# Performance work log

Measured on AMD Instinct MI355X. Metric: run time of the kernel, lower is better.

Reference implementation:

```python
import jax, jax.numpy as jnp
import numpy as np

NH = 8          # num_heads (init kwarg)
NUM_GROUPS = 32
EPS = 1e-5


def setup_inputs() -> dict:
    key = jax.random.key(0)
    ks = jax.random.split(key, 4)
    B, C, H, W = 2, 512, 64, 64
    x = jax.random.normal(ks[0], (B, C, H, W), dtype=jnp.float32)
    qkv_w = jax.random.normal(ks[1], (3 * C, C), dtype=jnp.float32) * (1.0 / np.sqrt(C))
    proj_w = jax.random.normal(ks[2], (C, C), dtype=jnp.float32) * (1.0 / np.sqrt(C))
    proj_b = jax.random.normal(ks[3], (C,), dtype=jnp.float32) * 0.02
    gn_w = jnp.ones((C,), dtype=jnp.float32)
    gn_b = jnp.zeros((C,), dtype=jnp.float32)
    return {"x": x, "qkv_w": qkv_w, "proj_w": proj_w, "proj_b": proj_b,
            "gn_w": gn_w, "gn_b": gn_b}


def _group_norm(x, gamma, beta):
    B, C, H, W = x.shape
    xg = x.reshape(B, NUM_GROUPS, C // NUM_GROUPS, H, W)
    mean = xg.mean(axis=(2, 3, 4), keepdims=True)
    var = xg.var(axis=(2, 3, 4), keepdims=True)
    xg = (xg - mean) * jax.lax.rsqrt(var + EPS)
    x = xg.reshape(B, C, H, W)
    return x * gamma[None, :, None, None] + beta[None, :, None, None]


def reference(x, qkv_w, proj_w, proj_b, gn_w, gn_b):
    B, C, H, W = x.shape
    h = _group_norm(x, gn_w, gn_b)
    # 1x1 conv == channel matmul
    qkv = jnp.einsum('oc,bchw->bohw', qkv_w, h)  # [B, 3C, H, W]
    # faithful legacy reshape: per-head contiguous [q,k,v] blocks of 3*C//NH channels
    qkv = qkv.reshape(B * NH, 3 * C // NH, H * W)
    q, k, v = jnp.split(qkv, 3, axis=1)          # each [B*NH, C//NH, HW]
    scale = 1.0 / np.sqrt(np.sqrt(C // NH))
    attn = jnp.einsum('bci,bcj->bij', q * scale, k * scale)  # [B*NH, HW, HW]
    attn = jax.nn.softmax(attn, axis=-1)
    hout = jnp.einsum('bij,bcj->bci', attn, v)   # [B*NH, C//NH, HW]
    hout = hout.reshape(B, C, H, W)
    hout = jnp.einsum('oc,bchw->bohw', proj_w, hout) + proj_b[None, :, None, None]
    return x + hout
```

## Files before the change

### kernel.cpp

```cpp
#include <hip/hip_runtime.h>
#include <math.h>

typedef __attribute__((ext_vector_type(8))) short short8;
typedef __attribute__((ext_vector_type(4))) float floatx4;

__device__ __forceinline__ unsigned short f2bf(float f) {
  union { float f; unsigned int u; } v; v.f = f;
  unsigned int r = v.u + 0x7fffu + ((v.u >> 16) & 1u);
  return (unsigned short)(r >> 16);
}

__device__ __forceinline__ unsigned int pack2(unsigned short a, unsigned short b) {
  return (unsigned int)a | ((unsigned int)b << 16);
}

__device__ __forceinline__ unsigned int rbits(float f) {
  union { float f; unsigned int u; } v; v.f = f;
  return v.u + 0x8000u;
}

__device__ __forceinline__ float fast_exp2(float x) {
#if __has_builtin(__builtin_amdgcn_exp2f)
  return __builtin_amdgcn_exp2f(x);
#else
  return exp2f(x);
#endif
}

__device__ __forceinline__ void async16(const unsigned short* gp, unsigned short* lp) {
  __builtin_amdgcn_global_load_lds(
      (__attribute__((address_space(1))) void*)(gp),
      (__attribute__((address_space(3))) void*)(lp), 16, 0, 0);
}

__global__ void gn_stats(const float* __restrict__ x, float* __restrict__ stats) {
  int bg = blockIdx.x;
  const float4* p = (const float4*)(x + (size_t)bg * 65536);
  float s = 0.f, ss = 0.f;
  for (int i = threadIdx.x; i < 16384; i += 256) {
    float4 v = p[i];
    s  += v.x + v.y + v.z + v.w;
    ss += v.x*v.x + v.y*v.y + v.z*v.z + v.w*v.w;
  }
  #pragma unroll
  for (int off = 32; off >= 1; off >>= 1) {
    s  += __shfl_xor(s,  off, 64);
    ss += __shfl_xor(ss, off, 64);
  }
  __shared__ float red[2][4];
  int wv = threadIdx.x >> 6;
  if ((threadIdx.x & 63) == 0) { red[0][wv] = s; red[1][wv] = ss; }
  __syncthreads();
  if (threadIdx.x == 0) {
    s  = red[0][0] + red[0][1] + red[0][2] + red[0][3];
    ss = red[1][0] + red[1][1] + red[1][2] + red[1][3];
    float mean = s * (1.f/65536.f);
    float var  = ss * (1.f/65536.f) - mean*mean;
    stats[2*bg]   = mean;
    stats[2*bg+1] = rsqrtf(var + 1e-5f);
  }
}

__global__ void gn_apply_t(const float* __restrict__ x, const float* __restrict__ stats,
                           const float* __restrict__ gw, const float* __restrict__ gb,
                           unsigned short* __restrict__ h_t) {
  __shared__ __align__(16) unsigned short tile[64][72];
  const int b = blockIdx.z, c0 = blockIdx.y * 64, hw0 = blockIdx.x * 64;
  const int t = threadIdx.x;
  {
    const int cl = t >> 2;
    const int hs = (t & 3) * 16;
    const int c  = c0 + cl;
    const int g  = c >> 4;
    const float mean = stats[2*(b*32 + g)];
    const float rstd = stats[2*(b*32 + g) + 1];
    const float w  = gw[c] * rstd;
    const float bb = gb[c] - mean * w;
    const float4* src = (const float4*)(x + ((size_t)(b*512 + c))*4096 + hw0 + hs);
    #pragma unroll
    for (int i = 0; i < 4; i++) {
      float4 vv = src[i];
      unsigned short* d = &tile[cl][hs + i*4];
      d[0] = f2bf(vv.x*w + bb); d[1] = f2bf(vv.y*w + bb);
      d[2] = f2bf(vv.z*w + bb); d[3] = f2bf(vv.w*w + bb);
    }
  }
  __syncthreads();
  {
    const int hwl = t >> 2;
    const int cs  = (t & 3) * 16;
    uint4 w0, w1;
    w0.x = pack2(tile[cs+ 0][hwl], tile[cs+ 1][hwl]);
    w0.y = pack2(tile[cs+ 2][hwl], tile[cs+ 3][hwl]);
    w0.z = pack2(tile[cs+ 4][hwl], tile[cs+ 5][hwl]);
    w0.w = pack2(tile[cs+ 6][hwl], tile[cs+ 7][hwl]);
    w1.x = pack2(tile[cs+ 8][hwl], tile[cs+ 9][hwl]);
    w1.y = pack2(tile[cs+10][hwl], tile[cs+11][hwl]);
    w1.z = pack2(tile[cs+12][hwl], tile[cs+13][hwl]);
    w1.w = pack2(tile[cs+14][hwl], tile[cs+15][hwl]);
    unsigned short* dst = h_t + ((size_t)(b*4096 + hw0 + hwl))*512 + c0 + cs;
    *(uint4*)dst       = w0;
    *(uint4*)(dst + 8) = w1;
  }
}

__global__ void castw(const float* __restrict__ src, unsigned short* __restrict__ dst, int n4) {
  int i = blockIdx.x * 256 + threadIdx.x;
  if (i < n4) {
    float4 vv = ((const float4*)src)[i];
    uint2 o;
    o.x = pack2(f2bf(vv.x), f2bf(vv.y));
    o.y = pack2(f2bf(vv.z), f2bf(vv.w));
    ((uint2*)dst)[i] = o;
  }
}

template <int MODE>
__global__ __launch_bounds__(256, 2)
void gemm_bt(const unsigned short* __restrict__ A,
             const unsigned short* __restrict__ Bt,
             unsigned short* __restrict__ q_t,
             unsigned short* __restrict__ k_t,
             unsigned short* __restrict__ v_,
             float* __restrict__ outp,
             const float* __restrict__ xres,
             const float* __restrict__ pbias) {
  __shared__ __align__(16) unsigned short As[128*32];
  __shared__ __align__(16) unsigned short Bs[128*32];
  const int b   = blockIdx.z;
  const int n0  = blockIdx.x * 128;
  const int o0  = blockIdx.y * 128;
  const int tid = threadIdx.x;
  const int wave = tid >> 6, lane = tid & 63;
  const int wr = wave >> 1, wc = wave & 1;
  const int fm = lane & 15, fq = lane >> 4;
  const int srow = lane >> 2, scol = (lane & 3) * 8;

  const unsigned short* Ab = A + (size_t)o0 * 512;
  const unsigned short* Bb = Bt + ((size_t)b*4096 + n0) * 512;

  floatx4 acc[4][4];
  #pragma unroll
  for (int i = 0; i < 4; i++)
    #pragma unroll
    for (int j = 0; j < 4; j++) acc[i][j] = (floatx4){0.f,0.f,0.f,0.f};

  for (int k0 = 0; k0 < 512; k0 += 32) {
    __syncthreads();
    #pragma unroll
    for (int cc = 0; cc < 2; cc++) {
      int ch = wave*2 + cc;
      async16(Ab + (size_t)(ch*16 + srow)*512 + k0 + scol, &As[ch*512]);
      async16(Bb + (size_t)(ch*16 + srow)*512 + k0 + scol, &Bs[ch*512]);
    }
    __syncthreads();
    short8 af[4], bf[4];
    #pragma unroll
    for (int f = 0; f < 4; f++) {
      af[f] = *(const short8*)&As[(wr*64 + f*16 + fm)*32 + fq*8];
      bf[f] = *(const short8*)&Bs[(wc*64 + f*16 + fm)*32 + fq*8];
    }
    #pragma unroll
    for (int fr = 0; fr < 4; fr++)
      #pragma unroll
      for (int fc = 0; fc < 4; fc++)
        acc[fr][fc] = __builtin_amdgcn_mfma_f32_16x16x32_bf16(af[fr], bf[fc], acc[fr][fc], 0, 0, 0);
  }

  if (MODE == 0) {
    #pragma unroll
    for (int fr = 0; fr < 4; fr++) {
      const int ob     = o0 + wr*64 + fr*16;
      const int head   = ob / 192;
      const int rem    = ob % 192;
      const int region = rem >> 6;
      const int dsub   = (rem & 63) + fq*4;
      const int bhh    = b*8 + head;
      #pragma unroll
      for (int fc = 0; fc < 4; fc++) {
        const int i = n0 + wc*64 + fc*16 + fm;
        if (region == 0) {
          unsigned short t4[4];
          #pragma unroll
          for (int r = 0; r < 4; r++) t4[r] = f2bf(acc[fr][fc][r] * 0.18033688f);
          uint2 o; o.x = pack2(t4[0], t4[1]); o.y = pack2(t4[2], t4[3]);
          *(uint2*)&q_t[((size_t)bhh*4096 + i)*64 + dsub] = o;
        } else if (region == 1) {
          unsigned short t4[4];
          #pragma unroll
          for (int r = 0; r < 4; r++) t4[r] = f2bf(acc[fr][fc][r]);
          uint2 o; o.x = pack2(t4[0], t4[1]); o.y = pack2(t4[2], t4[3]);
          *(uint2*)&k_t[((size_t)bhh*4096 + i)*64 + dsub] = o;
        } else {
          #pragma unroll
          for (int r = 0; r < 4; r++)
            v_[((size_t)bhh*64 + dsub + r)*4096 + i] = f2bf(acc[fr][fc][r]);
        }
      }
    }
  } else {
    #pragma unroll
    for (int fr = 0; fr < 4; fr++)
      #pragma unroll
      for (int fc = 0; fc < 4; fc++) {
        const int i = n0 + wc*64 + fc*16 + fm;
        #pragma unroll
        for (int r = 0; r < 4; r++) {
          const int o = o0 + wr*64 + fr*16 + fq*4 + r;
          const size_t idx = ((size_t)b*512 + o)*4096 + i;
          outp[idx] = xres[idx] + pbias[o] + acc[fr][fc][r];
        }
      }
  }
}

__global__ __launch_bounds__(256, 2)
void attn_kernel(const unsigned short* __restrict__ q_t,
                 const unsigned short* __restrict__ k_t,
                 const unsigned short* __restrict__ v_,
                 unsigned short* __restrict__ hout_t) {
  __shared__ __align__(16) unsigned short Ks[2][64*72];
  __shared__ __align__(16) unsigned short Vs[2][64*72];
  __shared__ __align__(16) unsigned short Ps[128*72];

  const int bh  = blockIdx.x;
  const int q0  = blockIdx.y * 128;
  const int tid = threadIdx.x;
  const int wave = tid >> 6, lane = tid & 63;
  const int fm = lane & 15, fq = lane >> 4;

  short8 qf[2][2];
  #pragma unroll
  for (int ih = 0; ih < 2; ih++) {
    const unsigned short* qrow = q_t + ((size_t)bh*4096 + q0 + wave*32 + ih*16 + fm)*64;
    qf[ih][0] = *(const short8*)(qrow + fq*8);
    qf[ih][1] = *(const short8*)(qrow + 32 + fq*8);
  }

  floatx4 o_acc[2][4];
  #pragma unroll
  for (int a = 0; a < 2; a++)
    #pragma unroll
    for (int d = 0; d < 4; d++) o_acc[a][d] = (floatx4){0.f,0.f,0.f,0.f};
  float l0 = 0.f, l1 = 0.f;

  const int sr = tid >> 3;
  const int sc = (tid & 7) * 8;
  const unsigned short* kbase = k_t + (size_t)bh*262144;
  const unsigned short* vbase = v_  + (size_t)bh*262144;
  unsigned short* Pw = &Ps[(wave*32)*72];

  uint4 kr0 = *(const uint4*)&kbase[(size_t)sr*64 + sc];
  uint4 kr1 = *(const uint4*)&kbase[(size_t)(sr+32)*64 + sc];
  uint4 vr0 = *(const uint4*)&vbase[(size_t)sr*4096 + sc];
  uint4 vr1 = *(const uint4*)&vbase[(size_t)(sr+32)*4096 + sc];

  for (int it = 0; it < 64; it++) {
    unsigned short* Kc = Ks[it & 1];
    unsigned short* Vc = Vs[it & 1];
    *(uint4*)&Kc[sr*72 + sc]      = kr0;
    *(uint4*)&Kc[(sr+32)*72 + sc] = kr1;
    *(uint4*)&Vc[sr*72 + sc]      = vr0;
    *(uint4*)&Vc[(sr+32)*72 + sc] = vr1;
    __syncthreads();

    {
      const int jn = ((it + 1) & 63) * 64;
      kr0 = *(const uint4*)&kbase[(size_t)(jn + sr)*64 + sc];
      kr1 = *(const uint4*)&kbase[(size_t)(jn + sr + 32)*64 + sc];
      vr0 = *(const uint4*)&vbase[(size_t)sr*4096 + jn + sc];
      vr1 = *(const uint4*)&vbase[(size_t)(sr+32)*4096 + jn + sc];
    }

    floatx4 s[4][2];
    #pragma unroll
    for (int jf = 0; jf < 4; jf++) {
      short8 kf0 = *(const short8*)&Kc[(jf*16 + fm)*72 + fq*8];
      short8 kf1 = *(const short8*)&Kc[(jf*16 + fm)*72 + 32 + fq*8];
      #pragma unroll
      for (int ih = 0; ih < 2; ih++) {
        floatx4 a = (floatx4){0.f,0.f,0.f,0.f};
        a = __builtin_amdgcn_mfma_f32_16x16x32_bf16(kf0, qf[ih][0], a, 0, 0, 0);
        a = __builtin_amdgcn_mfma_f32_16x16x32_bf16(kf1, qf[ih][1], a, 0, 0, 0);
        s[jf][ih] = a;
      }
    }

    #pragma unroll
    for (int jf = 0; jf < 4; jf++) {
      #pragma unroll
      for (int ih = 0; ih < 2; ih++) {
        float p0 = fast_exp2(s[jf][ih][0]);
        float p1 = fast_exp2(s[jf][ih][1]);
        float p2 = fast_exp2(s[jf][ih][2]);
        float p3 = fast_exp2(s[jf][ih][3]);
        if (ih) l1 += (p0 + p1) + (p2 + p3); else l0 += (p0 + p1) + (p2 + p3);
        uint2 w;
        w.x = __builtin_amdgcn_perm(rbits(p1), rbits(p0), 0x07060302u);
        w.y = __builtin_amdgcn_perm(rbits(p3), rbits(p2), 0x07060302u);
        *(uint2*)&Pw[(ih*16 + fm)*72 + jf*16 + fq*4] = w;
      }
    }

    #pragma unroll
    for (int jc = 0; jc < 2; jc++) {
      short8 pf0 = *(const short8*)&Pw[(fm)*72      + jc*32 + fq*8];
      short8 pf1 = *(const short8*)&Pw[(16 + fm)*72 + jc*32 + fq*8];
      #pragma unroll
      for (int df = 0; df < 4; df++) {
        short8 vf = *(const short8*)&Vc[(df*16 + fm)*72 + jc*32 + fq*8];
        o_acc[0][df] = __builtin_amdgcn_mfma_f32_16x16x32_bf16(pf0, vf, o_acc[0][df], 0, 0, 0);
        o_acc[1][df] = __builtin_amdgcn_mfma_f32_16x16x32_bf16(pf1, vf, o_acc[1][df], 0, 0, 0);
      }
    }
  }

  l0 += __shfl_xor(l0, 16, 64); l0 += __shfl_xor(l0, 32, 64);
  l1 += __shfl_xor(l1, 16, 64); l1 += __shfl_xor(l1, 32, 64);

  const int bb = bh >> 3;
  const int cb = (bh & 7) * 64;
  #pragma unroll
  for (int ih = 0; ih < 2; ih++) {
    #pragma unroll
    for (int r = 0; r < 4; r++) {
      const int src = (lane & 48) | (fq*4 + r);
      const float lv = __shfl(ih ? l1 : l0, src, 64);
      const float inv = 1.f / lv;
      const int i = q0 + wave*32 + ih*16 + fq*4 + r;
      #pragma unroll
      for (int df = 0; df < 4; df++)
        hout_t[((size_t)bb*4096 + i)*512 + cb + df*16 + fm] = f2bf(o_acc[ih][df][r] * inv);
    }
  }
}

extern "C" void kernel_launch(void* const* d_in, const int* in_sizes, int n_in,
                              void* d_out, int out_size, void* d_ws, size_t ws_size,
                              hipStream_t stream) {
  (void)in_sizes; (void)n_in; (void)out_size; (void)ws_size;
  const float* x      = (const float*)d_in[0];
  const float* qkv_w  = (const float*)d_in[1];
  const float* proj_w = (const float*)d_in[2];
  const float* proj_b = (const float*)d_in[3];
  const float* gn_w   = (const float*)d_in[4];
  const float* gn_b   = (const float*)d_in[5];
  float* out = (float*)d_out;

  char* ws = (char*)d_ws;
  unsigned short* h_t   = (unsigned short*)(ws);
  unsigned short* q_t   = (unsigned short*)(ws + ((size_t)8  << 20));
  unsigned short* k_t   = (unsigned short*)(ws + ((size_t)16 << 20));
  unsigned short* v_    = (unsigned short*)(ws + ((size_t)24 << 20));
  unsigned short* wqkv  = (unsigned short*)(ws + ((size_t)32 << 20));
  unsigned short* wproj = (unsigned short*)(ws + ((size_t)34 << 20));
  float* stats          = (float*)(ws + ((size_t)35 << 20));
  unsigned short* hout_t = h_t;

  gn_stats<<<dim3(64), dim3(256), 0, stream>>>(x, stats);
  gn_apply_t<<<dim3(64, 8, 2), dim3(256), 0, stream>>>(x, stats, gn_w, gn_b, h_t);
  castw<<<dim3(768), dim3(256), 0, stream>>>(qkv_w, wqkv, 196608);
  castw<<<dim3(256), dim3(256), 0, stream>>>(proj_w, wproj, 65536);
  gemm_bt<0><<<dim3(32, 12, 2), dim3(256), 0, stream>>>(wqkv, h_t, q_t, k_t, v_,
                                                        nullptr, nullptr, nullptr);
  attn_kernel<<<dim3(16, 32), dim3(256), 0, stream>>>(q_t, k_t, v_, hout_t);
  gemm_bt<1><<<dim3(32, 4, 2), dim3(256), 0, stream>>>(wproj, hout_t,
                                                       nullptr, nullptr, nullptr,
                                                       out, x, proj_b);
}
```

Before: 227.3 us.

## Use 32x32 MFMA in attention with register-resident P, vectorize V stores, merge weight casts

The attention inner loop now uses 32x32x16 MFMA for QK^T and keeps the exponentiated scores in registers, feeding them directly as the A operand of 32x32x8 MFMAs for PV. This drops the shared-memory P buffer along with its write/read round trip and cuts LDS traffic per iteration. In the QKV GEMM, the V region swaps the MFMA operands so each lane holds contiguous tokens and can issue packed 8-byte stores instead of scattered 2-byte ones. The two weight-cast launches are merged into one. The larger accumulators increase register pressure, which could hurt occupancy.

```diff
diff --git a/kernel.cpp b/kernel.cpp
--- a/kernel.cpp
+++ b/kernel.cpp
@@ -2,7 +2,9 @@
 #include <math.h>
 
 typedef __attribute__((ext_vector_type(8))) short short8;
+typedef __attribute__((ext_vector_type(4))) short short4v;
 typedef __attribute__((ext_vector_type(4))) float floatx4;
+typedef __attribute__((ext_vector_type(16))) float floatx16;
 
 __device__ __forceinline__ unsigned short f2bf(float f) {
   union { float f; unsigned int u; } v; v.f = f;
@@ -104,15 +106,17 @@
   }
 }
 
-__global__ void castw(const float* __restrict__ src, unsigned short* __restrict__ dst, int n4) {
+__global__ void castw2(const float* __restrict__ sa, unsigned short* __restrict__ da, int n4a,
+                       const float* __restrict__ sb, unsigned short* __restrict__ db) {
   int i = blockIdx.x * 256 + threadIdx.x;
-  if (i < n4) {
-    float4 vv = ((const float4*)src)[i];
-    uint2 o;
-    o.x = pack2(f2bf(vv.x), f2bf(vv.y));
-    o.y = pack2(f2bf(vv.z), f2bf(vv.w));
-    ((uint2*)dst)[i] = o;
-  }
+  const float* s; unsigned short* d;
+  if (i < n4a) { s = sa; d = da; }
+  else { i -= n4a; s = sb; d = db; }
+  float4 vv = ((const float4*)s)[i];
+  uint2 o;
+  o.x = pack2(f2bf(vv.x), f2bf(vv.y));
+  o.y = pack2(f2bf(vv.z), f2bf(vv.w));
+  ((uint2*)d)[i] = o;
 }
 
 template <int MODE>
@@ -139,6 +143,13 @@
   const unsigned short* Ab = A + (size_t)o0 * 512;
   const unsigned short* Bb = Bt + ((size_t)b*4096 + n0) * 512;
 
+  bool vsw[4];
+  #pragma unroll
+  for (int fr = 0; fr < 4; fr++) {
+    const int ob = o0 + wr*64 + fr*16;
+    vsw[fr] = (MODE == 0) && ((ob % 192) >> 6) == 2;
+  }
+
   floatx4 acc[4][4];
   #pragma unroll
   for (int i = 0; i < 4; i++)
@@ -161,10 +172,17 @@
       bf[f] = *(const short8*)&Bs[(wc*64 + f*16 + fm)*32 + fq*8];
     }
     #pragma unroll
-    for (int fr = 0; fr < 4; fr++)
-      #pragma unroll
-      for (int fc = 0; fc < 4; fc++)
-        acc[fr][fc] = __builtin_amdgcn_mfma_f32_16x16x32_bf16(af[fr], bf[fc], acc[fr][fc], 0, 0, 0);
+    for (int fr = 0; fr < 4; fr++) {
+      if (vsw[fr]) {
+        #pragma unroll
+        for (int fc = 0; fc < 4; fc++)
+          acc[fr][fc] = __builtin_amdgcn_mfma_f32_16x16x32_bf16(bf[fc], af[fr], acc[fr][fc], 0, 0, 0);
+      } else {
+        #pragma unroll
+        for (int fc = 0; fc < 4; fc++)
+          acc[fr][fc] = __builtin_amdgcn_mfma_f32_16x16x32_bf16(af[fr], bf[fc], acc[fr][fc], 0, 0, 0);
+      }
+    }
   }
 
   if (MODE == 0) {
@@ -174,27 +192,33 @@
       const int head   = ob / 192;
       const int rem    = ob % 192;
       const int region = rem >> 6;
-      const int dsub   = (rem & 63) + fq*4;
       const int bhh    = b*8 + head;
       #pragma unroll
       for (int fc = 0; fc < 4; fc++) {
-        const int i = n0 + wc*64 + fc*16 + fm;
         if (region == 0) {
+          const int i = n0 + wc*64 + fc*16 + fm;
+          const int dsub = (rem & 63) + fq*4;
           unsigned short t4[4];
           #pragma unroll
           for (int r = 0; r < 4; r++) t4[r] = f2bf(acc[fr][fc][r] * 0.18033688f);
           uint2 o; o.x = pack2(t4[0], t4[1]); o.y = pack2(t4[2], t4[3]);
           *(uint2*)&q_t[((size_t)bhh*4096 + i)*64 + dsub] = o;
         } else if (region == 1) {
+          const int i = n0 + wc*64 + fc*16 + fm;
+          const int dsub = (rem & 63) + fq*4;
           unsigned short t4[4];
           #pragma unroll
           for (int r = 0; r < 4; r++) t4[r] = f2bf(acc[fr][fc][r]);
           uint2 o; o.x = pack2(t4[0], t4[1]); o.y = pack2(t4[2], t4[3]);
           *(uint2*)&k_t[((size_t)bhh*4096 + i)*64 + dsub] = o;
         } else {
+          const int dsub = (rem & 63) + fm;
+          const int tok0 = n0 + wc*64 + fc*16 + fq*4;
+          unsigned short t4[4];
           #pragma unroll
-          for (int r = 0; r < 4; r++)
-            v_[((size_t)bhh*64 + dsub + r)*4096 + i] = f2bf(acc[fr][fc][r]);
+          for (int r = 0; r < 4; r++) t4[r] = f2bf(acc[fr][fc][r]);
+          uint2 o; o.x = pack2(t4[0], t4[1]); o.y = pack2(t4[2], t4[3]);
+          *(uint2*)&v_[((size_t)bhh*64 + dsub)*4096 + tok0] = o;
         }
       }
     }
@@ -221,34 +245,32 @@
                  unsigned short* __restrict__ hout_t) {
   __shared__ __align__(16) unsigned short Ks[2][64*72];
   __shared__ __align__(16) unsigned short Vs[2][64*72];
-  __shared__ __align__(16) unsigned short Ps[128*72];
 
   const int bh  = blockIdx.x;
   const int q0  = blockIdx.y * 128;
   const int tid = threadIdx.x;
   const int wave = tid >> 6, lane = tid & 63;
-  const int fm = lane & 15, fq = lane >> 4;
-
-  short8 qf[2][2];
-  #pragma unroll
-  for (int ih = 0; ih < 2; ih++) {
-    const unsigned short* qrow = q_t + ((size_t)bh*4096 + q0 + wave*32 + ih*16 + fm)*64;
-    qf[ih][0] = *(const short8*)(qrow + fq*8);
-    qf[ih][1] = *(const short8*)(qrow + 32 + fq*8);
-  }
-
-  floatx4 o_acc[2][4];
-  #pragma unroll
-  for (int a = 0; a < 2; a++)
-    #pragma unroll
-    for (int d = 0; d < 4; d++) o_acc[a][d] = (floatx4){0.f,0.f,0.f,0.f};
-  float l0 = 0.f, l1 = 0.f;
+  const int ln = lane & 31, h = lane >> 5;
+
+  short8 qf[4];
+  {
+    const unsigned short* qrow = q_t + ((size_t)bh*4096 + q0 + wave*32 + ln)*64;
+    #pragma unroll
+    for (int kc = 0; kc < 4; kc++)
+      qf[kc] = *(const short8*)(qrow + kc*16 + h*8);
+  }
+
+  floatx16 o_acc[2];
+  #pragma unroll
+  for (int dn = 0; dn < 2; dn++)
+    #pragma unroll
+    for (int r = 0; r < 16; r++) o_acc[dn][r] = 0.f;
+  float l = 0.f;
 
   const int sr = tid >> 3;
   const int sc = (tid & 7) * 8;
   const unsigned short* kbase = k_t + (size_t)bh*262144;
   const unsigned short* vbase = v_  + (size_t)bh*262144;
-  unsigned short* Pw = &Ps[(wave*32)*72];
 
   uint4 kr0 = *(const uint4*)&kbase[(size_t)sr*64 + sc];
   uint4 kr1 = *(const uint4*)&kbase[(size_t)(sr+32)*64 + sc];
@@ -272,66 +294,59 @@
       vr1 = *(const uint4*)&vbase[(size_t)(sr+32)*4096 + jn + sc];
     }
 
-    floatx4 s[4][2];
-    #pragma unroll
-    for (int jf = 0; jf < 4; jf++) {
-      short8 kf0 = *(const short8*)&Kc[(jf*16 + fm)*72 + fq*8];
-      short8 kf1 = *(const short8*)&Kc[(jf*16 + fm)*72 + 32 + fq*8];
-      #pragma unroll
-      for (int ih = 0; ih < 2; ih++) {
-        floatx4 a = (floatx4){0.f,0.f,0.f,0.f};
-        a = __builtin_amdgcn_mfma_f32_16x16x32_bf16(kf0, qf[ih][0], a, 0, 0, 0);
-        a = __builtin_amdgcn_mfma_f32_16x16x32_bf16(kf1, qf[ih][1], a, 0, 0, 0);
-        s[jf][ih] = a;
-      }
-    }
-
-    #pragma unroll
-    for (int jf = 0; jf < 4; jf++) {
-      #pragma unroll
-      for (int ih = 0; ih < 2; ih++) {
-        float p0 = fast_exp2(s[jf][ih][0]);
-        float p1 = fast_exp2(s[jf][ih][1]);
-        float p2 = fast_exp2(s[jf][ih][2]);
-        float p3 = fast_exp2(s[jf][ih][3]);
-        if (ih) l1 += (p0 + p1) + (p2 + p3); else l0 += (p0 + p1) + (p2 + p3);
-        uint2 w;
-        w.x = __builtin_amdgcn_perm(rbits(p1), rbits(p0), 0x07060302u);
-        w.y = __builtin_amdgcn_perm(rbits(p3), rbits(p2), 0x07060302u);
-        *(uint2*)&Pw[(ih*16 + fm)*72 + jf*16 + fq*4] = w;
-      }
-    }
-
-    #pragma unroll
-    for (int jc = 0; jc < 2; jc++) {
-      short8 pf0 = *(const short8*)&Pw[(fm)*72      + jc*32 + fq*8];
-      short8 pf1 = *(const short8*)&Pw[(16 + fm)*72 + jc*32 + fq*8];
-      #pragma unroll
-      for (int df = 0; df < 4; df++) {
-        short8 vf = *(const short8*)&Vc[(df*16 + fm)*72 + jc*32 + fq*8];
-        o_acc[0][df] = __builtin_amdgcn_mfma_f32_16x16x32_bf16(pf0, vf, o_acc[0][df], 0, 0, 0);
-        o_acc[1][df] = __builtin_amdgcn_mfma_f32_16x16x32_bf16(pf1, vf, o_acc[1][df], 0, 0, 0);
-      }
-    }
-  }
-
-  l0 += __shfl_xor(l0, 16, 64); l0 += __shfl_xor(l0, 32, 64);
-  l1 += __shfl_xor(l1, 16, 64); l1 += __shfl_xor(l1, 32, 64);
+    floatx16 st[2];
+    #pragma unroll
+    for (int mj = 0; mj < 2; mj++) {
+      #pragma unroll
+      for (int r = 0; r < 16; r++) st[mj][r] = 0.f;
+      #pragma unroll
+      for (int kc = 0; kc < 4; kc++) {
+        short8 kA = *(const short8*)&Kc[(mj*32 + ln)*72 + kc*16 + h*8];
+        st[mj] = __builtin_amdgcn_mfma_f32_32x32x16_bf16(kA, qf[kc], st[mj], 0, 0, 0);
+      }
+    }
+
+    unsigned pk[2][8];
+    #pragma unroll
+    for (int mj = 0; mj < 2; mj++) {
+      #pragma unroll
+      for (int rp = 0; rp < 8; rp++) {
+        float p0 = fast_exp2(st[mj][2*rp]);
+        float p1 = fast_exp2(st[mj][2*rp + 1]);
+        l += p0 + p1;
+        pk[mj][rp] = __builtin_amdgcn_perm(rbits(p1), rbits(p0), 0x07060302u);
+      }
+    }
+
+    #pragma unroll
+    for (int mj = 0; mj < 2; mj++) {
+      #pragma unroll
+      for (int t = 0; t < 4; t++) {
+        union { unsigned u[2]; short4v s; } uu;
+        uu.u[0] = pk[mj][2*t]; uu.u[1] = pk[mj][2*t + 1];
+        const short4v af = uu.s;
+        #pragma unroll
+        for (int dn = 0; dn < 2; dn++) {
+          const short4v vf = *(const short4v*)&Vc[(dn*32 + ln)*72 + mj*32 + t*8 + h*4];
+          o_acc[dn] = __builtin_amdgcn_mfma_f32_32x32x8bf16_1k(af, vf, o_acc[dn], 0, 0, 0);
+        }
+      }
+    }
+  }
+
+  l += __shfl_xor(l, 32, 64);
+  const float linv = 1.f / l;
 
   const int bb = bh >> 3;
   const int cb = (bh & 7) * 64;
   #pragma unroll
-  for (int ih = 0; ih < 2; ih++) {
-    #pragma unroll
-    for (int r = 0; r < 4; r++) {
-      const int src = (lane & 48) | (fq*4 + r);
-      const float lv = __shfl(ih ? l1 : l0, src, 64);
-      const float inv = 1.f / lv;
-      const int i = q0 + wave*32 + ih*16 + fq*4 + r;
-      #pragma unroll
-      for (int df = 0; df < 4; df++)
-        hout_t[((size_t)bb*4096 + i)*512 + cb + df*16 + fm] = f2bf(o_acc[ih][df][r] * inv);
-    }
+  for (int r = 0; r < 16; r++) {
+    const int il = (r & 3) + 8*(r >> 2) + 4*h;
+    const float inv = __shfl(linv, il, 64);
+    const int i = q0 + wave*32 + il;
+    unsigned short* dst = &hout_t[((size_t)bb*4096 + i)*512 + cb + ln];
+    dst[0]  = f2bf(o_acc[0][r] * inv);
+    dst[32] = f2bf(o_acc[1][r] * inv);
   }
 }
 
@@ -359,8 +374,7 @@
 
   gn_stats<<<dim3(64), dim3(256), 0, stream>>>(x, stats);
   gn_apply_t<<<dim3(64, 8, 2), dim3(256), 0, stream>>>(x, stats, gn_w, gn_b, h_t);
-  castw<<<dim3(768), dim3(256), 0, stream>>>(qkv_w, wqkv, 196608);
-  castw<<<dim3(256), dim3(256), 0, stream>>>(proj_w, wproj, 65536);
+  castw2<<<dim3(1024), dim3(256), 0, stream>>>(qkv_w, wqkv, 196608, proj_w, wproj);
   gemm_bt<0><<<dim3(32, 12, 2), dim3(256), 0, stream>>>(wqkv, h_t, q_t, k_t, v_,
                                                         nullptr, nullptr, nullptr);
   attn_kernel<<<dim3(16, 32), dim3(256), 0, stream>>>(q_t, k_t, v_, hout_t);
```

Measured after the change: 233.4 us. 2.7% more time.
